# Optimization experiments

Measured on AMD Instinct MI355X. Metric: run time of the kernel, lower is better.

Reference implementation:

```python
import jax, jax.numpy as jnp
import numpy as np

N_FILTERS = 1024
KH, KW = 5, 5
LOC = 3                      # locality (pad + maxpool kernel/stride)
B, H, W = 1024, 64, 64
WIN = KH + 2 * LOC           # 11: sliced window side after padding


def setup_inputs() -> dict:
    key = jax.random.key(0)
    k1, k2, k3, k4 = jax.random.split(key, 4)
    X = jax.random.normal(k1, (B, 1, H, W), dtype=jnp.float32)
    weight = jax.random.normal(k2, (N_FILTERS, 1, KH, KW), dtype=jnp.float32)
    bias = jax.random.normal(k3, (N_FILTERS,), dtype=jnp.float32)
    # top-left corner (i, j) of each filter's window in the padded image;
    # must satisfy i + KH + 2*LOC <= H + 2*LOC  =>  i in [0, H-KH]
    positions = jax.random.randint(k4, (N_FILTERS, 2), 0, H - KH + 1, dtype=jnp.int32)
    return {"X": X, "weight": weight, "bias": bias, "positions": positions}


def reference(X, weight, bias, positions):
    # ZeroPad2d(locality)
    Xp = jnp.pad(X, ((0, 0), (0, 0), (LOC, LOC), (LOC, LOC)))

    def slice_one(pos):
        return jax.lax.dynamic_slice(Xp, (0, 0, pos[0], pos[1]), (B, 1, WIN, WIN))

    windows = jax.vmap(slice_one)(positions)
    lhs = jnp.transpose(windows[:, :, 0], (1, 0, 2, 3))

    # All n_filters tiny single-channel convs as ONE grouped conv.
    conv = jax.lax.conv_general_dilated(
        lhs, weight, window_strides=(1, 1), padding='VALID',
        dimension_numbers=('NCHW', 'OIHW', 'NCHW'),
        feature_group_count=N_FILTERS)                # [B,F,2L+1,2L+1] = [B,F,7,7]
    conv = conv + bias[None, :, None, None]

    # MaxPool2d((LOC,LOC)) with default stride=LOC, floor mode -> 2x2.
    pooled = jax.lax.reduce_window(
        conv, -jnp.inf, jax.lax.max,
        window_dimensions=(1, 1, LOC, LOC),
        window_strides=(1, 1, LOC, LOC),
        padding='VALID')                              # [B,F,2,2]

    # torch.cat(dim=1) over per-filter [B,1,2,2] tensors + reshape(B,-1)
    return pooled.reshape(B, -1)                      # [B, F*4]
```

## Files before the change

kernel.cpp:

```cpp
#include <hip/hip_runtime.h>

#define N_FILTERS 1024
#define B_TOTAL   1024
#define IMG       64
#define PAD_DIM   70

typedef _Float16 half2_t __attribute__((ext_vector_type(2)));

__global__ void zero_border_kernel(_Float16* __restrict__ Xt) {
    int pp = blockIdx.x;
    int r = pp / PAD_DIM, c = pp - r * PAD_DIM;
    if (r >= 3 && r < 67 && c >= 3 && c < 67) return;
    unsigned int* q = (unsigned int*)Xt + (size_t)pp * 512;
    q[threadIdx.x] = 0u;
    q[threadIdx.x + 256] = 0u;
}

__global__ __launch_bounds__(256) void transpose_kernel(
    const float* __restrict__ X, _Float16* __restrict__ Xt)
{
    __shared__ float T[64 * 65];
    const int pt = blockIdx.x & 63;
    const int bt = blockIdx.x >> 6;
    const int tx = threadIdx.x & 63, ty = threadIdx.x >> 6;

    #pragma unroll
    for (int pass = 0; pass < 16; ++pass) {
        int bl = pass * 4 + ty;
        T[bl * 65 + tx] = X[(size_t)(bt * 64 + bl) * 4096 + pt * 64 + tx];
    }
    __syncthreads();
    #pragma unroll
    for (int pass = 0; pass < 16; ++pass) {
        int pl = pass * 4 + ty;
        int p  = pt * 64 + pl;
        int r  = p >> 6, c = p & 63;
        Xt[(size_t)((r + 3) * PAD_DIM + (c + 3)) * 1024 + bt * 64 + tx]
            = (_Float16)T[tx * 65 + pl];
    }
}

__global__ void filters_main(
    const half2_t* __restrict__ Xt2,
    const float*   __restrict__ W,
    const float*   __restrict__ bias,
    const int*     __restrict__ pos,
    float4*        __restrict__ out4)
{
    const int t    = threadIdx.x;
    const int lane = t & 63;
    const int w    = t >> 6;
    const int bg   = blockIdx.x & 7;
    const int fg   = blockIdx.x >> 3;

    const int f  = fg * 4 + w;
    const int sf = __builtin_amdgcn_readfirstlane(f);
    const int si = __builtin_amdgcn_readfirstlane(pos[2 * sf]);
    const int sj = __builtin_amdgcn_readfirstlane(pos[2 * sf + 1]);

    float wk[25];
    const float* wp = W + sf * 25;
    #pragma unroll
    for (int k = 0; k < 25; ++k) wk[k] = wp[k];

    const int pb = bg * 64 + lane;

    float accA[36], accB[36];
    #pragma unroll
    for (int k = 0; k < 36; ++k) { accA[k] = 0.0f; accB[k] = 0.0f; }

    #pragma unroll
    for (int wr = 0; wr < 10; ++wr) {
        const half2_t* rowp = Xt2 + (size_t)((si + wr) * PAD_DIM + sj) * 512 + pb;
        float inA[10], inB[10];
        #pragma unroll
        for (int wc = 0; wc < 10; ++wc) {
            half2_t h = rowp[(size_t)wc * 512];
            inA[wc] = (float)h.x;
            inB[wc] = (float)h.y;
        }
        #pragma unroll
        for (int y = 0; y < 6; ++y) {
            if (y >= ((wr > 4) ? (wr - 4) : 0) && y <= ((wr < 5) ? wr : 5)) {
                const int r = wr - y;
                #pragma unroll
                for (int x = 0; x < 6; ++x) {
                    #pragma unroll
                    for (int c = 0; c < 5; ++c) {
                        accA[y * 6 + x] = fmaf(wk[r * 5 + c], inA[x + c], accA[y * 6 + x]);
                        accB[y * 6 + x] = fmaf(wk[r * 5 + c], inB[x + c], accB[y * 6 + x]);
                    }
                }
            }
        }
    }

    const float bv = bias[sf];
    float4 oA, oB;
    {
        float mA[4], mB[4];
        #pragma unroll
        for (int py = 0; py < 2; ++py) {
            #pragma unroll
            for (int px = 0; px < 2; ++px) {
                float a = accA[(3 * py) * 6 + 3 * px];
                float b = accB[(3 * py) * 6 + 3 * px];
                #pragma unroll
                for (int dy = 0; dy < 3; ++dy)
                    #pragma unroll
                    for (int dx = 0; dx < 3; ++dx) {
                        a = fmaxf(a, accA[(3 * py + dy) * 6 + (3 * px + dx)]);
                        b = fmaxf(b, accB[(3 * py + dy) * 6 + (3 * px + dx)]);
                    }
                mA[py * 2 + px] = a + bv;
                mB[py * 2 + px] = b + bv;
            }
        }
        oA.x = mA[0]; oA.y = mA[1]; oA.z = mA[2]; oA.w = mA[3];
        oB.x = mB[0]; oB.y = mB[1]; oB.z = mB[2]; oB.w = mB[3];
    }

    const int b = bg * 128 + lane * 2;
    out4[(size_t)b * 1024 + f]       = oA;
    out4[(size_t)(b + 1) * 1024 + f] = oB;
}

extern "C" void kernel_launch(void* const* d_in, const int* in_sizes, int n_in,
                              void* d_out, int out_size, void* d_ws, size_t ws_size,
                              hipStream_t stream) {
    const float* X    = (const float*)d_in[0];
    const float* W    = (const float*)d_in[1];
    const float* bias = (const float*)d_in[2];
    const int*   pos  = (const int*)d_in[3];
    float4* out4 = (float4*)d_out;
    _Float16* Xt = (_Float16*)d_ws;

    zero_border_kernel<<<PAD_DIM * PAD_DIM, 256, 0, stream>>>(Xt);
    transpose_kernel<<<1024, 256, 0, stream>>>(X, Xt);
    filters_main<<<2048, 256, 0, stream>>>((const half2_t*)Xt, W, bias, pos, out4);
}
```

Before: 110.9 us.

## Fuse border-zero into transpose and process four batch elements per lane with packed FMA

Merges the border-zeroing and transpose kernels into one launch, with dedicated blocks handling the zero border. The transpose now handles 128 batch elements per block and writes half2 pairs. The main kernel gives each lane four batch elements loaded as 8-byte vectors and accumulates in float2 vectors, so the compiler can emit packed FP32 FMAs (v_pk_fma_f32), and it halves the grid. The cost is roughly double the accumulator register pressure (144 floats), with launch bounds asking for 2 blocks per CU, so register spilling or lower occupancy is a risk.

```diff
diff --git a/kernel.cpp b/kernel.cpp
--- a/kernel.cpp
+++ b/kernel.cpp
@@ -6,52 +6,57 @@
 #define PAD_DIM   70
 
 typedef _Float16 half2_t __attribute__((ext_vector_type(2)));
+typedef float    fvec2   __attribute__((ext_vector_type(2)));
 
-__global__ void zero_border_kernel(_Float16* __restrict__ Xt) {
-    int pp = blockIdx.x;
-    int r = pp / PAD_DIM, c = pp - r * PAD_DIM;
-    if (r >= 3 && r < 67 && c >= 3 && c < 67) return;
-    unsigned int* q = (unsigned int*)Xt + (size_t)pp * 512;
-    q[threadIdx.x] = 0u;
-    q[threadIdx.x + 256] = 0u;
-}
-
-__global__ __launch_bounds__(256) void transpose_kernel(
+__global__ __launch_bounds__(256) void prep_kernel(
     const float* __restrict__ X, _Float16* __restrict__ Xt)
 {
-    __shared__ float T[64 * 65];
-    const int pt = blockIdx.x & 63;
-    const int bt = blockIdx.x >> 6;
-    const int tx = threadIdx.x & 63, ty = threadIdx.x >> 6;
+    if (blockIdx.x < 512) {
+        __shared__ float T[128 * 65];
+        const int pt = blockIdx.x & 63;
+        const int bt = blockIdx.x >> 6;
+        const int tx = threadIdx.x & 63, ty = threadIdx.x >> 6;
 
-    #pragma unroll
-    for (int pass = 0; pass < 16; ++pass) {
-        int bl = pass * 4 + ty;
-        T[bl * 65 + tx] = X[(size_t)(bt * 64 + bl) * 4096 + pt * 64 + tx];
-    }
-    __syncthreads();
-    #pragma unroll
-    for (int pass = 0; pass < 16; ++pass) {
-        int pl = pass * 4 + ty;
-        int p  = pt * 64 + pl;
-        int r  = p >> 6, c = p & 63;
-        Xt[(size_t)((r + 3) * PAD_DIM + (c + 3)) * 1024 + bt * 64 + tx]
-            = (_Float16)T[tx * 65 + pl];
+        #pragma unroll
+        for (int pass = 0; pass < 32; ++pass) {
+            int bl = pass * 4 + ty;
+            T[bl * 65 + tx] = X[(size_t)(bt * 128 + bl) * 4096 + pt * 64 + tx];
+        }
+        __syncthreads();
+        #pragma unroll
+        for (int pass = 0; pass < 16; ++pass) {
+            int pl = pass * 4 + ty;
+            int p  = pt * 64 + pl;
+            int r  = p >> 6, c = p & 63;
+            half2_t h;
+            h.x = (_Float16)T[(2 * tx) * 65 + pl];
+            h.y = (_Float16)T[(2 * tx + 1) * 65 + pl];
+            *(half2_t*)&Xt[(size_t)((r + 3) * PAD_DIM + (c + 3)) * 1024 + bt * 128 + 2 * tx] = h;
+        }
+    } else {
+        const int bp = blockIdx.x - 512;
+        for (int pp = bp; pp < PAD_DIM * PAD_DIM; pp += 64) {
+            int r = pp / PAD_DIM, c = pp - r * PAD_DIM;
+            if (r >= 3 && r < 67 && c >= 3 && c < 67) continue;
+            unsigned int* q = (unsigned int*)Xt + (size_t)pp * 512;
+            q[threadIdx.x] = 0u;
+            q[threadIdx.x + 256] = 0u;
+        }
     }
 }
 
-__global__ void filters_main(
-    const half2_t* __restrict__ Xt2,
-    const float*   __restrict__ W,
-    const float*   __restrict__ bias,
-    const int*     __restrict__ pos,
-    float4*        __restrict__ out4)
+__global__ __launch_bounds__(256, 2) void filters_main(
+    const _Float16* __restrict__ Xt,
+    const float*    __restrict__ W,
+    const float*    __restrict__ bias,
+    const int*      __restrict__ pos,
+    float4*         __restrict__ out4)
 {
     const int t    = threadIdx.x;
     const int lane = t & 63;
     const int w    = t >> 6;
-    const int bg   = blockIdx.x & 7;
-    const int fg   = blockIdx.x >> 3;
+    const int bg   = blockIdx.x & 3;
+    const int fg   = blockIdx.x >> 2;
 
     const int f  = fg * 4 + w;
     const int sf = __builtin_amdgcn_readfirstlane(f);
@@ -63,21 +68,25 @@
     #pragma unroll
     for (int k = 0; k < 25; ++k) wk[k] = wp[k];
 
-    const int pb = bg * 64 + lane;
+    const int laneByte = bg * 512 + lane * 8;
 
-    float accA[36], accB[36];
+    fvec2 a0[36], a1[36];
     #pragma unroll
-    for (int k = 0; k < 36; ++k) { accA[k] = 0.0f; accB[k] = 0.0f; }
+    for (int k = 0; k < 36; ++k) { a0[k] = (fvec2)0.0f; a1[k] = (fvec2)0.0f; }
 
     #pragma unroll
     for (int wr = 0; wr < 10; ++wr) {
-        const half2_t* rowp = Xt2 + (size_t)((si + wr) * PAD_DIM + sj) * 512 + pb;
-        float inA[10], inB[10];
+        const char* rowp = (const char*)Xt
+                         + (size_t)((si + wr) * PAD_DIM + sj) * 2048 + laneByte;
+        fvec2 inA[10], inB[10];
         #pragma unroll
         for (int wc = 0; wc < 10; ++wc) {
-            half2_t h = rowp[(size_t)wc * 512];
-            inA[wc] = (float)h.x;
-            inB[wc] = (float)h.y;
+            half2_t lo, hi;
+            uint2 d = *(const uint2*)(rowp + (size_t)wc * 2048);
+            lo = __builtin_bit_cast(half2_t, d.x);
+            hi = __builtin_bit_cast(half2_t, d.y);
+            inA[wc].x = (float)lo.x; inA[wc].y = (float)lo.y;
+            inB[wc].x = (float)hi.x; inB[wc].y = (float)hi.y;
         }
         #pragma unroll
         for (int y = 0; y < 6; ++y) {
@@ -87,8 +96,8 @@
                 for (int x = 0; x < 6; ++x) {
                     #pragma unroll
                     for (int c = 0; c < 5; ++c) {
-                        accA[y * 6 + x] = fmaf(wk[r * 5 + c], inA[x + c], accA[y * 6 + x]);
-                        accB[y * 6 + x] = fmaf(wk[r * 5 + c], inB[x + c], accB[y * 6 + x]);
+                        a0[y * 6 + x] = wk[r * 5 + c] * inA[x + c] + a0[y * 6 + x];
+                        a1[y * 6 + x] = wk[r * 5 + c] * inB[x + c] + a1[y * 6 + x];
                     }
                 }
             }
@@ -96,33 +105,40 @@
     }
 
     const float bv = bias[sf];
-    float4 oA, oB;
+    float4 o0, o1;
     {
-        float mA[4], mB[4];
+        fvec2 m0[4], m1[4];
         #pragma unroll
         for (int py = 0; py < 2; ++py) {
             #pragma unroll
             for (int px = 0; px < 2; ++px) {
-                float a = accA[(3 * py) * 6 + 3 * px];
-                float b = accB[(3 * py) * 6 + 3 * px];
+                fvec2 u = a0[(3 * py) * 6 + 3 * px];
+                fvec2 v = a1[(3 * py) * 6 + 3 * px];
                 #pragma unroll
                 for (int dy = 0; dy < 3; ++dy)
                     #pragma unroll
                     for (int dx = 0; dx < 3; ++dx) {
-                        a = fmaxf(a, accA[(3 * py + dy) * 6 + (3 * px + dx)]);
-                        b = fmaxf(b, accB[(3 * py + dy) * 6 + (3 * px + dx)]);
+                        fvec2 e0 = a0[(3 * py + dy) * 6 + (3 * px + dx)];
+                        fvec2 e1 = a1[(3 * py + dy) * 6 + (3 * px + dx)];
+                        u.x = fmaxf(u.x, e0.x); u.y = fmaxf(u.y, e0.y);
+                        v.x = fmaxf(v.x, e1.x); v.y = fmaxf(v.y, e1.y);
                     }
-                mA[py * 2 + px] = a + bv;
-                mB[py * 2 + px] = b + bv;
+                m0[py * 2 + px].x = u.x + bv; m0[py * 2 + px].y = u.y + bv;
+                m1[py * 2 + px].x = v.x + bv; m1[py * 2 + px].y = v.y + bv;
             }
         }
-        oA.x = mA[0]; oA.y = mA[1]; oA.z = mA[2]; oA.w = mA[3];
-        oB.x = mB[0]; oB.y = mB[1]; oB.z = mB[2]; oB.w = mB[3];
+        const int b0 = bg * 256 + lane * 4;
+        float4 o;
+        o.x = m0[0].x; o.y = m0[1].x; o.z = m0[2].x; o.w = m0[3].x;
+        out4[(size_t)b0 * 1024 + f] = o;
+        o.x = m0[0].y; o.y = m0[1].y; o.z = m0[2].y; o.w = m0[3].y;
+        out4[(size_t)(b0 + 1) * 1024 + f] = o;
+        o.x = m1[0].x; o.y = m1[1].x; o.z = m1[2].x; o.w = m1[3].x;
+        out4[(size_t)(b0 + 2) * 1024 + f] = o;
+        o.x = m1[0].y; o.y = m1[1].y; o.z = m1[2].y; o.w = m1[3].y;
+        out4[(size_t)(b0 + 3) * 1024 + f] = o;
+        (void)o0; (void)o1;
     }
-
-    const int b = bg * 128 + lane * 2;
-    out4[(size_t)b * 1024 + f]       = oA;
-    out4[(size_t)(b + 1) * 1024 + f] = oB;
 }
 
 extern "C" void kernel_launch(void* const* d_in, const int* in_sizes, int n_in,
@@ -135,7 +151,6 @@
     float4* out4 = (float4*)d_out;
     _Float16* Xt = (_Float16*)d_ws;
 
-    zero_border_kernel<<<PAD_DIM * PAD_DIM, 256, 0, stream>>>(Xt);
-    transpose_kernel<<<1024, 256, 0, stream>>>(X, Xt);
-    filters_main<<<2048, 256, 0, stream>>>((const half2_t*)Xt, W, bias, pos, out4);
+    prep_kernel<<<576, 256, 0, stream>>>(X, Xt);
+    filters_main<<<1024, 256, 0, stream>>>(Xt, W, bias, pos, out4);
 }
```

Measured after the change: 104.1 us. -6.1%, faster.
